# Optimization experiments

Measured on AMD Instinct MI355X. Metric: run time of the kernel, lower is better.

## Reference

```python
import jax, jax.numpy as jnp
import numpy as np

TWO_PI = 2.0 * np.pi


def quat2mat3(q):
    # q: (B,4) (w,x,y,z), normalized internally -> (B,3,3)
    q = q / jnp.linalg.norm(q, axis=-1, keepdims=True)
    w, x, y, z = q[:, 0], q[:, 1], q[:, 2], q[:, 3]
    R = jnp.stack([
        1 - 2 * (y * y + z * z), 2 * (x * y - w * z), 2 * (x * z + w * y),
        2 * (x * y + w * z), 1 - 2 * (x * x + z * z), 2 * (y * z - w * x),
        2 * (x * z - w * y), 2 * (y * z + w * x), 1 - 2 * (x * x + y * y),
    ], axis=-1).reshape(-1, 3, 3)
    return R


def se3(R, t):
    # R: (B,3,3), t: (B,3) -> (B,4,4)
    B = R.shape[0]
    top = jnp.concatenate([R, t[:, :, None]], axis=2)            # (B,3,4)
    bottom = jnp.broadcast_to(jnp.array([[0., 0., 0., 1.]], R.dtype), (B, 1, 4))
    return jnp.concatenate([top, bottom], axis=1)


def mat2quat(R):
    # batched rotation matrix -> quaternion (w,x,y,z), branchless 4-case Shepperd
    R00, R01, R02 = R[:, 0, 0], R[:, 0, 1], R[:, 0, 2]
    R10, R11, R12 = R[:, 1, 0], R[:, 1, 1], R[:, 1, 2]
    R20, R21, R22 = R[:, 2, 0], R[:, 2, 1], R[:, 2, 2]
    tr = R00 + R11 + R22
    t0 = 1.0 + tr
    t1 = 1.0 + R00 - R11 - R22
    t2 = 1.0 - R00 + R11 - R22
    t3 = 1.0 - R00 - R11 + R22
    q0 = jnp.stack([t0, R21 - R12, R02 - R20, R10 - R01], axis=-1)
    q1 = jnp.stack([R21 - R12, t1, R01 + R10, R02 + R20], axis=-1)
    q2 = jnp.stack([R02 - R20, R01 + R10, t2, R12 + R21], axis=-1)
    q3 = jnp.stack([R10 - R01, R02 + R20, R12 + R21, t3], axis=-1)
    qs = jnp.stack([q0, q1, q2, q3], axis=1)   # (B,4,4)
    ts = jnp.stack([t0, t1, t2, t3], axis=1)   # (B,4)
    diag = jnp.stack([R00, R11, R22], axis=1)
    sel = jnp.where(tr > 0, 0, 1 + jnp.argmax(diag, axis=1))
    q = jnp.take_along_axis(qs, sel[:, None, None].astype(jnp.int32).repeat(4, 2), axis=1)[:, 0]
    t = jnp.take_along_axis(ts, sel[:, None].astype(jnp.int32), axis=1)[:, 0]
    return q * (0.5 / jnp.sqrt(jnp.clip(t, 1e-12)))[:, None]


def quat_mul(a, b):
    aw, av = a[:, :1], a[:, 1:]
    bw, bv = b[:, :1], b[:, 1:]
    w = aw * bw - jnp.sum(av * bv, axis=1, keepdims=True)
    v = aw * bv + bw * av + jnp.cross(av, bv)
    return jnp.concatenate([w, v], axis=1)


def quat_distance(q, r):
    r_inv = jnp.concatenate([r[:, :1], -r[:, 1:]], axis=1)  # conjugate (unit quats)
    d = quat_mul(q, r_inv)
    return 2.0 * jnp.arctan2(jnp.linalg.norm(d[:, 1:], axis=1), jnp.abs(d[:, 0]))


def smooth_l1(x, y):
    d = jnp.abs(x - y)
    return jnp.where(d < 1.0, 0.5 * d * d, d - 0.5)


def _rand_se3(key, B):
    kq, kt = jax.random.split(key)
    q = jax.random.normal(kq, (B, 4), jnp.float32)
    R = quat2mat3(q)
    t = jax.random.normal(kt, (B, 3), jnp.float32)
    return se3(R, t)


def setup_inputs() -> dict:
    key = jax.random.key(0)
    B, N = 8, 1_000_000
    k1, k2, k3, k4, k5 = jax.random.split(key, 5)
    return {
        "pred_translation": 0.1 * jax.random.normal(k1, (B, 3), jnp.float32),
        "pred_rotation": jax.random.normal(k2, (B, 4), jnp.float32),
        "pcs": 20.0 * jax.random.normal(k3, (B, N, 3), jnp.float32),
        "gt_T_to_camera": _rand_se3(k4, B),
        "init_T_to_camera": _rand_se3(k5, B),
        "mask": jnp.ones((B, N), jnp.int32),
    }


def reference(pred_translation, pred_rotation, pcs, gt_T_to_camera, init_T_to_camera, mask):
    W_T, W_R, W_PC, W_QN = 1.0, 0.5, 0.5, 0.5
    B = pcs.shape[0]

    # quat norm loss on raw predicted quaternion
    norm_sq = jnp.sum(pred_rotation ** 2, axis=1)
    qn_loss = jnp.mean((norm_sq - 1.0) ** 2)

    # T_pred = trans(t) @ rot(q)  -> (B,4,4)
    T_t = se3(jnp.broadcast_to(jnp.eye(3, dtype=pcs.dtype), (B, 3, 3)), pred_translation)
    T_r = se3(quat2mat3(pred_rotation), jnp.zeros((B, 3), pcs.dtype))
    T_pred = jnp.einsum('bij,bjk->bik', T_t, T_r)

    # T_gt_expected = inv(T_pred) @ init_T
    T_gt_exp = jnp.einsum('bij,bjk->bik', jnp.linalg.inv(T_pred), init_T_to_camera)
    p_t = T_gt_exp[:, :3, 3]
    p_R = T_gt_exp[:, :3, :3]
    g_t = gt_T_to_camera[:, :3, 3]
    g_R = gt_T_to_camera[:, :3, :3]

    # translation: smooth-L1, sum over axes, mean over batch
    t_loss = jnp.mean(jnp.sum(smooth_l1(p_t, g_t), axis=1))

    # PC reprojection: RT_total = inv(gt_T) @ [p_R|p_t]
    T_pred2 = se3(p_R, p_t)
    RT = jnp.einsum('bij,bjk->bik', jnp.linalg.inv(gt_T_to_camera), T_pred2)
    pts = jnp.einsum('bij,bnj->bni', RT[:, :3, :3], pcs) + RT[:, None, :3, 3]
    err = jnp.linalg.norm(pts - pcs, axis=2)               # (B,N)
    mf = mask.astype(pcs.dtype)
    pc_loss = jnp.mean(jnp.sum(err * mf, axis=1) / jnp.sum(mf, axis=1))

    # rotation: quaternion geodesic distance between matrix-derived quats
    r_loss = jnp.mean(quat_distance(mat2quat(p_R), mat2quat(g_R)))

    loss = W_T * t_loss + W_R * r_loss + W_PC * pc_loss + W_QN * qn_loss
    return loss
```

## Files before the change

### kernel.cpp

```cpp
#include <hip/hip_runtime.h>
#include <math.h>

struct Pose {
    float M[9], Tt[3], pR[9], pt[3], gR[9], gt[3], qn;
};

__device__ __forceinline__ float smooth_l1f(float x, float y) {
    float d = fabsf(x - y);
    return d < 1.0f ? 0.5f * d * d : d - 0.5f;
}

__device__ void mat2quat_dev(const float* R, float* q) {
    float R00=R[0],R01=R[1],R02=R[2];
    float R10=R[3],R11=R[4],R12=R[5];
    float R20=R[6],R21=R[7],R22=R[8];
    float tr = R00 + R11 + R22;
    float t;
    if (tr > 0.0f) {
        t = 1.0f + tr;
        q[0]=t; q[1]=R21-R12; q[2]=R02-R20; q[3]=R10-R01;
    } else {
        int sel = 1; float best = R00;
        if (R11 > best) { sel = 2; best = R11; }
        if (R22 > best) { sel = 3; }
        if (sel == 1)      { t = 1.0f+R00-R11-R22; q[0]=R21-R12; q[1]=t; q[2]=R01+R10; q[3]=R02+R20; }
        else if (sel == 2) { t = 1.0f-R00+R11-R22; q[0]=R02-R20; q[1]=R01+R10; q[2]=t; q[3]=R12+R21; }
        else               { t = 1.0f-R00-R11+R22; q[0]=R10-R01; q[1]=R02+R20; q[2]=R12+R21; q[3]=t; }
    }
    float s = 0.5f / sqrtf(fmaxf(t, 1e-12f));
    q[0]*=s; q[1]*=s; q[2]*=s; q[3]*=s;
}

__device__ void compute_pose(int b,
                             const float* __restrict__ pred_t,
                             const float* __restrict__ pred_q,
                             const float* __restrict__ gtT,
                             const float* __restrict__ initT,
                             Pose& P)
{
    float tx=pred_t[b*3+0], ty=pred_t[b*3+1], tz=pred_t[b*3+2];
    float q0=pred_q[b*4+0], q1=pred_q[b*4+1], q2=pred_q[b*4+2], q3=pred_q[b*4+3];
    float nsq = q0*q0+q1*q1+q2*q2+q3*q3;
    P.qn = (nsq-1.0f)*(nsq-1.0f);
    float inv = rsqrtf(nsq);
    float w=q0*inv, x=q1*inv, y=q2*inv, z=q3*inv;
    float R[9];
    R[0]=1.0f-2.0f*(y*y+z*z); R[1]=2.0f*(x*y-w*z);      R[2]=2.0f*(x*z+w*y);
    R[3]=2.0f*(x*y+w*z);      R[4]=1.0f-2.0f*(x*x+z*z); R[5]=2.0f*(y*z-w*x);
    R[6]=2.0f*(x*z-w*y);      R[7]=2.0f*(y*z+w*x);      R[8]=1.0f-2.0f*(x*x+y*y);

    float iR[9], it[3];
    for (int i=0;i<3;i++){
        for (int j=0;j<3;j++){
            iR[i*3+j]=initT[b*16+i*4+j];
            P.gR[i*3+j]=gtT[b*16+i*4+j];
        }
        it[i]=initT[b*16+i*4+3];
        P.gt[i]=gtT[b*16+i*4+3];
    }
    for (int i=0;i<3;i++){
        for (int j=0;j<3;j++)
            P.pR[i*3+j] = R[0+i]*iR[0+j] + R[3+i]*iR[3+j] + R[6+i]*iR[6+j];
        P.pt[i] = R[0+i]*(it[0]-tx) + R[3+i]*(it[1]-ty) + R[6+i]*(it[2]-tz);
    }
    for (int i=0;i<3;i++){
        for (int j=0;j<3;j++)
            P.M[i*3+j] = P.gR[0+i]*P.pR[0+j] + P.gR[3+i]*P.pR[3+j] + P.gR[6+i]*P.pR[6+j];
        P.Tt[i] = P.gR[0+i]*(P.pt[0]-P.gt[0]) + P.gR[3+i]*(P.pt[1]-P.gt[1]) + P.gR[6+i]*(P.pt[2]-P.gt[2]);
    }
    P.M[0]-=1.0f; P.M[4]-=1.0f; P.M[8]-=1.0f;
}

#define TP  512
#define F4T 384
#define M4T 128

__global__ __launch_bounds__(256) void pc_fused(const float* __restrict__ pcs,
                                                const int* __restrict__ mask,
                                                const float* __restrict__ pred_t,
                                                const float* __restrict__ pred_q,
                                                const float* __restrict__ gtT,
                                                const float* __restrict__ initT,
                                                float* __restrict__ errS,
                                                float* __restrict__ maskS,
                                                int N, int bpb, int chunk)
{
    int b   = blockIdx.x / bpb;
    int blk = blockIdx.x - b*bpb;
    int t   = threadIdx.x;

    __shared__ float sMT[12];
    __shared__ float sP[2][F4T*4];
    __shared__ float sK[2][TP];
    __shared__ float sE[4], sM[4];

    int r0 = blk * chunk;
    if (r0 >= N) {
        if (t==0){ errS[blockIdx.x]=0.0f; maskS[blockIdx.x]=0.0f; }
        return;
    }
    int my_pts = N - r0; if (my_pts > chunk) my_pts = chunk;
    int nt    = (my_pts + TP - 1) / TP;
    int my_f4 = (my_pts * 3) >> 2;
    int my_m4 = my_pts >> 2;

    const float4* pf4 = (const float4*)pcs  + ((size_t)b*N + r0)*3/4;
    const int4*   mi4 = (const int4*)  mask + ((size_t)b*N + r0)/4;

    if (t == 0) {
        Pose P;
        compute_pose(b, pred_t, pred_q, gtT, initT, P);
        #pragma unroll
        for (int k=0;k<9;k++) sMT[k]=P.M[k];
        sMT[9]=P.Tt[0]; sMT[10]=P.Tt[1]; sMT[11]=P.Tt[2];
    }

    float4 rA = make_float4(0,0,0,0);
    float4 rB = make_float4(0,0,0,0);
    float4 rM = make_float4(0,0,0,0);

    auto stage = [&](int ti) {
        int fbase = ti * F4T;
        bool full = (ti*TP + TP <= my_pts);
        if (full) {
            rA = pf4[fbase + t];
            if (t < 128) {
                rB = pf4[fbase + 256 + t];
                int4 m = mi4[ti*M4T + t];
                rM = make_float4((float)m.x,(float)m.y,(float)m.z,(float)m.w);
            }
        } else {
            int s0 = fbase + t;
            rA = (s0 < my_f4) ? pf4[s0] : make_float4(0,0,0,0);
            if (t < 128) {
                int s1 = fbase + 256 + t;
                rB = (s1 < my_f4) ? pf4[s1] : make_float4(0,0,0,0);
                int s2 = ti*M4T + t;
                if (s2 < my_m4) {
                    int4 m = mi4[s2];
                    rM = make_float4((float)m.x,(float)m.y,(float)m.z,(float)m.w);
                } else rM = make_float4(0,0,0,0);
            }
        }
    };
    auto wr = [&](int buf) {
        ((float4*)sP[buf])[t] = rA;
        if (t < 128) {
            ((float4*)sP[buf])[256 + t] = rB;
            ((float4*)sK[buf])[t]       = rM;
        }
    };

    stage(0);
    __syncthreads();
    float m00=sMT[0], m01=sMT[1], m02=sMT[2];
    float m10=sMT[3], m11=sMT[4], m12=sMT[5];
    float m20=sMT[6], m21=sMT[7], m22=sMT[8];
    float t0 =sMT[9], t1 =sMT[10], t2 =sMT[11];
    wr(0);
    __syncthreads();

    float esum = 0.0f, msum = 0.0f;
    for (int ti = 0; ti < nt; ti++) {
        int cur = ti & 1;
        if (ti + 1 < nt) stage(ti + 1);
        #pragma unroll
        for (int k = 0; k < 2; k++) {
            int p = t + (k << 8);
            float x = sP[cur][3*p], y = sP[cur][3*p+1], z = sP[cur][3*p+2];
            float mm = sK[cur][p];
            float dx = fmaf(m00,x, fmaf(m01,y, fmaf(m02,z, t0)));
            float dy = fmaf(m10,x, fmaf(m11,y, fmaf(m12,z, t1)));
            float dz = fmaf(m20,x, fmaf(m21,y, fmaf(m22,z, t2)));
            esum = fmaf(mm, sqrtf(fmaf(dx,dx, fmaf(dy,dy, dz*dz))), esum);
            msum += mm;
        }
        if (ti + 1 < nt) wr(cur ^ 1);
        __syncthreads();
    }

    for (int off=32; off>0; off>>=1){
        esum += __shfl_down(esum, off);
        msum += __shfl_down(msum, off);
    }
    int lane = t & 63, wid = t >> 6;
    if (lane==0){ sE[wid]=esum; sM[wid]=msum; }
    __syncthreads();
    if (t==0){
        errS [blockIdx.x] = sE[0]+sE[1]+sE[2]+sE[3];
        maskS[blockIdx.x] = sM[0]+sM[1]+sM[2]+sM[3];
    }
}

__global__ void finish_kernel(const float* __restrict__ errS,
                              const float* __restrict__ maskS,
                              const float* __restrict__ pred_t,
                              const float* __restrict__ pred_q,
                              const float* __restrict__ gtT,
                              const float* __restrict__ initT,
                              float* __restrict__ out, int B, int bpb)
{
    int t = threadIdx.x, lane = t & 63, w = t >> 6;
    __shared__ double sPC[4];
    double acc = 0.0;
    for (int b = w; b < B; b += 4) {
        float e=0.0f, m=0.0f;
        for (int k=lane; k<bpb; k+=64){ e += errS[b*bpb+k]; m += maskS[b*bpb+k]; }
        for (int off=32; off>0; off>>=1){
            e += __shfl_down(e, off);
            m += __shfl_down(m, off);
        }
        if (lane==0) acc += (double)e / (double)m;
    }
    if (lane==0) sPC[w] = acc;

    float partial = 0.0f;
    if (t < B) {
        Pose P;
        compute_pose(t, pred_t, pred_q, gtT, initT, P);
        float t_term = smooth_l1f(P.pt[0],P.gt[0]) + smooth_l1f(P.pt[1],P.gt[1])
                     + smooth_l1f(P.pt[2],P.gt[2]);
        float qp[4], qg[4];
        mat2quat_dev(P.pR,qp); mat2quat_dev(P.gR,qg);
        float dw  = qp[0]*qg[0] + qp[1]*qg[1] + qp[2]*qg[2] + qp[3]*qg[3];
        float cx  = qp[2]*qg[3]-qp[3]*qg[2];
        float cy  = qp[3]*qg[1]-qp[1]*qg[3];
        float cz  = qp[1]*qg[2]-qp[2]*qg[1];
        float dvx = -qp[0]*qg[1] + qg[0]*qp[1] - cx;
        float dvy = -qp[0]*qg[2] + qg[0]*qp[2] - cy;
        float dvz = -qp[0]*qg[3] + qg[0]*qp[3] - cz;
        float r_term = 2.0f*atan2f(sqrtf(dvx*dvx+dvy*dvy+dvz*dvz), fabsf(dw));
        partial = (1.0f*t_term + 0.5f*r_term + 0.5f*P.qn) / (float)B;
    }
    if (w==0)
        for (int off=32; off>0; off>>=1) partial += __shfl_down(partial, off);
    __syncthreads();
    if (t==0){
        double pc = sPC[0]+sPC[1]+sPC[2]+sPC[3];
        out[0] = partial + 0.5f * (float)(pc / (double)B);
    }
}

extern "C" void kernel_launch(void* const* d_in, const int* in_sizes, int n_in,
                              void* d_out, int out_size, void* d_ws, size_t ws_size,
                              hipStream_t stream)
{
    const float* pred_t = (const float*)d_in[0];
    const float* pred_q = (const float*)d_in[1];
    const float* pcs    = (const float*)d_in[2];
    const float* gtT    = (const float*)d_in[3];
    const float* initT  = (const float*)d_in[4];
    const int*   mask   = (const int*)d_in[5];

    int B = in_sizes[0] / 3;
    int N = in_sizes[2] / (B * 3);

    int bpb   = 256;
    int chunk = (((N + bpb - 1) / bpb) + 3) & ~3;

    float* errS  = (float*)d_ws;
    float* maskS = errS + B*bpb;
    float* out   = (float*)d_out;

    pc_fused<<<B*bpb, 256, 0, stream>>>(pcs, mask, pred_t, pred_q, gtT, initT,
                                        errS, maskS, N, bpb, chunk);
    finish_kernel<<<1, 256, 0, stream>>>(errS, maskS, pred_t, pred_q, gtT, initT,
                                         out, B, bpb);
}
```

Measured before the change: 31.07 us.

## Process four contiguous points per thread with register-held mask and larger tiles

Doubles the per-iteration tile to 1024 points so each of the 256 threads loads three float4s of coordinates and one int4 of mask. Each thread then reads its four consecutive points from shared memory as three float4s and keeps the mask in registers, which removes the mask shared buffer and the idle half-warp loads. Blocks per batch drop from 256 to 192, so each block handles more points with fewer launch and reduction partials. The trade-offs are higher register pressure and possible shared-memory bank conflicts from the stride-3 float4 reads.

```diff
diff --git a/kernel.cpp b/kernel.cpp
--- a/kernel.cpp
+++ b/kernel.cpp
@@ -71,9 +71,8 @@
     P.M[0]-=1.0f; P.M[4]-=1.0f; P.M[8]-=1.0f;
 }
 
-#define TP  512
-#define F4T 384
-#define M4T 128
+#define TP  1024
+#define F4T 768
 
 __global__ __launch_bounds__(256) void pc_fused(const float* __restrict__ pcs,
                                                 const int* __restrict__ mask,
@@ -91,7 +90,6 @@
 
     __shared__ float sMT[12];
     __shared__ float sP[2][F4T*4];
-    __shared__ float sK[2][TP];
     __shared__ float sE[4], sM[4];
 
     int r0 = blk * chunk;
@@ -117,38 +115,29 @@
 
     float4 rA = make_float4(0,0,0,0);
     float4 rB = make_float4(0,0,0,0);
-    float4 rM = make_float4(0,0,0,0);
+    float4 rC = make_float4(0,0,0,0);
+    int4   rM = make_int4(0,0,0,0);
 
     auto stage = [&](int ti) {
-        int fbase = ti * F4T;
-        bool full = (ti*TP + TP <= my_pts);
-        if (full) {
-            rA = pf4[fbase + t];
-            if (t < 128) {
-                rB = pf4[fbase + 256 + t];
-                int4 m = mi4[ti*M4T + t];
-                rM = make_float4((float)m.x,(float)m.y,(float)m.z,(float)m.w);
-            }
+        int fb = ti * F4T;
+        if (ti*TP + TP <= my_pts) {
+            rA = pf4[fb       + t];
+            rB = pf4[fb + 256 + t];
+            rC = pf4[fb + 512 + t];
+            rM = mi4[ti*256 + t];
         } else {
-            int s0 = fbase + t;
+            int s0 = fb + t, s1 = fb + 256 + t, s2 = fb + 512 + t, sm = ti*256 + t;
             rA = (s0 < my_f4) ? pf4[s0] : make_float4(0,0,0,0);
-            if (t < 128) {
-                int s1 = fbase + 256 + t;
-                rB = (s1 < my_f4) ? pf4[s1] : make_float4(0,0,0,0);
-                int s2 = ti*M4T + t;
-                if (s2 < my_m4) {
-                    int4 m = mi4[s2];
-                    rM = make_float4((float)m.x,(float)m.y,(float)m.z,(float)m.w);
-                } else rM = make_float4(0,0,0,0);
-            }
+            rB = (s1 < my_f4) ? pf4[s1] : make_float4(0,0,0,0);
+            rC = (s2 < my_f4) ? pf4[s2] : make_float4(0,0,0,0);
+            rM = (sm < my_m4) ? mi4[sm] : make_int4(0,0,0,0);
         }
     };
     auto wr = [&](int buf) {
-        ((float4*)sP[buf])[t] = rA;
-        if (t < 128) {
-            ((float4*)sP[buf])[256 + t] = rB;
-            ((float4*)sK[buf])[t]       = rM;
-        }
+        float4* d = (float4*)sP[buf];
+        d[t      ] = rA;
+        d[t + 256] = rB;
+        d[t + 512] = rC;
     };
 
     stage(0);
@@ -163,18 +152,24 @@
     float esum = 0.0f, msum = 0.0f;
     for (int ti = 0; ti < nt; ti++) {
         int cur = ti & 1;
+        int4 cM = rM;
         if (ti + 1 < nt) stage(ti + 1);
+
+        const float4* sp4 = (const float4*)sP[cur];
+        float4 A = sp4[3*t], C = sp4[3*t+1], D = sp4[3*t+2];
+        float px[4] = {A.x, A.w, C.z, D.y};
+        float py[4] = {A.y, C.x, C.w, D.z};
+        float pz[4] = {A.z, C.y, D.x, D.w};
+        float mf[4] = {(float)cM.x, (float)cM.y, (float)cM.z, (float)cM.w};
         #pragma unroll
-        for (int k = 0; k < 2; k++) {
-            int p = t + (k << 8);
-            float x = sP[cur][3*p], y = sP[cur][3*p+1], z = sP[cur][3*p+2];
-            float mm = sK[cur][p];
-            float dx = fmaf(m00,x, fmaf(m01,y, fmaf(m02,z, t0)));
-            float dy = fmaf(m10,x, fmaf(m11,y, fmaf(m12,z, t1)));
-            float dz = fmaf(m20,x, fmaf(m21,y, fmaf(m22,z, t2)));
-            esum = fmaf(mm, sqrtf(fmaf(dx,dx, fmaf(dy,dy, dz*dz))), esum);
-            msum += mm;
-        }
+        for (int j=0;j<4;j++){
+            float dx = fmaf(m00,px[j], fmaf(m01,py[j], fmaf(m02,pz[j], t0)));
+            float dy = fmaf(m10,px[j], fmaf(m11,py[j], fmaf(m12,pz[j], t1)));
+            float dz = fmaf(m20,px[j], fmaf(m21,py[j], fmaf(m22,pz[j], t2)));
+            esum = fmaf(mf[j], sqrtf(fmaf(dx,dx, fmaf(dy,dy, dz*dz))), esum);
+            msum += mf[j];
+        }
+
         if (ti + 1 < nt) wr(cur ^ 1);
         __syncthreads();
     }
@@ -255,7 +250,7 @@
     int B = in_sizes[0] / 3;
     int N = in_sizes[2] / (B * 3);
 
-    int bpb   = 256;
+    int bpb   = 192;
     int chunk = (((N + bpb - 1) / bpb) + 3) & ~3;
 
     float* errS  = (float*)d_ws;
```

Measured after the change: 31.36 us. No clear change (+1.0%).
